# Optimization experiments

Hardware: AMD Instinct MI355X
Metric: run time of the kernel (lower is better)

The kernel has to match this reference:

```python
import jax, jax.numpy as jnp
import numpy as np

BIG_K = 13
EPS = 1e-5  # torch BatchNorm2d default


def setup_inputs() -> dict:
    key = jax.random.key(0)
    k1, k2, k3, k4 = jax.random.split(key, 4)
    B, C1, C2, H, W_ = 8, 256, 256, 64, 64
    x = jax.random.normal(k1, (B, C1, H, W_), dtype=jnp.float32)
    # scale kernel by fan-in so pre-BN activations are O(1)
    fan_in = C1 * BIG_K * BIG_K
    W = jax.random.normal(k2, (C2, C1, BIG_K, BIG_K), dtype=jnp.float32) / np.sqrt(fan_in)
    gamma = jnp.ones((C2,), dtype=jnp.float32)
    beta = jnp.zeros((C2,), dtype=jnp.float32)
    running_mean = jax.random.normal(k3, (C2,), dtype=jnp.float32) * 0.1
    running_var = jax.random.uniform(k4, (C2,), dtype=jnp.float32, minval=0.5, maxval=1.5)
    return {"x": x, "W": W, "gamma": gamma, "beta": beta,
            "running_mean": running_mean, "running_var": running_var}


def reference(x, W, gamma, beta, running_mean, running_var):
    # Fallback path of ShiftWiseConv: big-kernel conv (no bias) -> BN (inference) -> SiLU
    pad = BIG_K // 2
    y = jax.lax.conv_general_dilated(
        x, W,
        window_strides=(1, 1),
        padding=[(pad, pad), (pad, pad)],
        dimension_numbers=("NCHW", "OIHW", "NCHW"),
    )
    inv = gamma * jax.lax.rsqrt(running_var + EPS)  # [C2]
    y = y * inv[None, :, None, None] + (beta - running_mean * inv)[None, :, None, None]
    return jax.nn.silu(y)
```

## Files before the change

kernel.cpp:

```cpp
#include <hip/hip_runtime.h>
#include <stdint.h>

#define EPS 1e-5f

typedef __attribute__((ext_vector_type(8))) __bf16 bf16x8;
typedef __attribute__((ext_vector_type(16))) float f32x16;

__device__ __forceinline__ int swz4(int r) { return (r ^ (r >> 2)) & 3; }

__device__ __forceinline__ unsigned short f2bf(float f) {
  union { float f; unsigned u; } v; v.f = f;
  unsigned r = v.u + 0x7fffu + ((v.u >> 16) & 1u);
  return (unsigned short)(r >> 16);
}

__device__ __forceinline__ void glds16(const unsigned short* g, unsigned short* l) {
  __builtin_amdgcn_global_load_lds(
      (const __attribute__((address_space(1))) void*)g,
      (__attribute__((address_space(3))) void*)l, 16, 0, 0);
}
__device__ __forceinline__ void glds4(const unsigned short* g, unsigned short* l) {
  __builtin_amdgcn_global_load_lds(
      (const __attribute__((address_space(1))) void*)g,
      (__attribute__((address_space(3))) void*)l, 4, 0, 0);
}

template <int N>
__device__ __forceinline__ void vmwait() {
  asm volatile("s_waitcnt vmcnt(%0)" ::"n"(N) : "memory");
}

__global__ __launch_bounds__(256) void pack_w_kernel(
    const float* __restrict__ W, unsigned short* __restrict__ Wp) {
  const int blk = blockIdx.x;
  const int c2 = blk / 13, kh = blk - c2 * 13;
  const int c1 = threadIdx.x;
  const int c2t = c2 >> 7, m = c2 & 127;
  const int c1c = c1 >> 5, c1i = c1 & 31;
  const float* src = W + (((size_t)(c2 * 256 + c1)) * 13 + kh) * 13;
  const int rowoff = (((c1i >> 3) ^ swz4(m)) << 3) + (c1i & 7);
#pragma unroll
  for (int kw = 0; kw < 13; ++kw) {
    const int ks = (kh * 8 + c1c) * 13 + kw;
    const size_t dst = (((size_t)c2t * 1352 + ks) * 128 + m) * 32 + rowoff;
    Wp[dst] = f2bf(src[kw]);
  }
}

__global__ __launch_bounds__(256) void pack_xt_kernel(
    const float* __restrict__ x, unsigned short* __restrict__ xT) {
  const int blk = blockIdx.x;
  const int rowp = blk % 76;
  const int bc = blk / 76;
  const int c1c = bc & 7, b = bc >> 3;
  const int row = rowp - 6;
  const bool rok = (unsigned)row < 64u;
  unsigned short* dst = xT + (size_t)blk * 2560;
  const float* srcb = x + (size_t)(b * 256 + c1c * 32) * 4096 +
                      (rok ? row * 64 : 0);
#pragma unroll
  for (int e = 0; e < 10; ++e) {
    const int idx = e * 256 + threadIdx.x;
    const int colp = idx >> 5, c1i = idx & 31;
    const int ic = colp - 8;
    const float v = (rok && (unsigned)ic < 64u) ? srcb[(size_t)c1i * 4096 + ic] : 0.f;
    dst[colp * 32 + ((((c1i >> 3) ^ swz4(colp)) << 3)) + (c1i & 7)] = f2bf(v);
  }
}

__global__ __launch_bounds__(256, 2) void conv10_kernel(
    const unsigned short* __restrict__ Wp, const unsigned short* __restrict__ xT,
    const float* __restrict__ gamma, const float* __restrict__ beta,
    const float* __restrict__ mean, const float* __restrict__ var,
    float* __restrict__ out) {
  __shared__ __align__(16) unsigned short Abuf[3][8192];
  __shared__ __align__(16) unsigned short Wbuf[2][5120];
  __shared__ float s_scale[128], s_shift[128];

  const int tid = threadIdx.x;
  const int bid = blockIdx.x;
  const int b = bid & 7;
  const int h0 = ((bid >> 3) & 31) * 2;
  const int c2t = bid >> 8;

  const int wid = tid >> 6, lane = tid & 63;
  const int wr = wid >> 1, wc = wid & 1;
  const int l31 = lane & 31, hi2 = lane >> 5;

  if (tid < 128) {
    const int c2 = c2t * 128 + tid;
    const float inv = gamma[c2] * rsqrtf(var[c2] + EPS);
    s_scale[tid] = inv;
    s_shift[tid] = beta[c2] - mean[c2] * inv;
  }

  int aoffs[2][2];
#pragma unroll
  for (int mt = 0; mt < 2; ++mt)
#pragma unroll
    for (int ks = 0; ks < 2; ++ks) {
      const int m = wr * 64 + mt * 32 + l31;
      aoffs[mt][ks] = m * 64 + (((ks * 2 + hi2) ^ swz4(m)) << 4);
    }
  int ndh[2], nwl[2];
#pragma unroll
  for (int nt = 0; nt < 2; ++nt) {
    const int n = wc * 64 + nt * 32 + l31;
    ndh[nt] = n >> 6;
    nwl[nt] = n & 63;
  }

  const int tid8 = tid * 8, tid2 = tid * 2;
  const int widA = wid * 512, wid128 = wid * 128;

  const size_t c2base = (size_t)c2t * 1352;
  const int bc8 = b * 8;
  const char* Abase = (const char*)&Abuf[0][0];
  unsigned short* AbaseU = &Abuf[0][0];

  auto wtile = [&](int T) -> const unsigned short* {
    const int kh = T >> 3, c1c = T & 7;
    return xT + (size_t)((bc8 + c1c) * 76 + h0 + kh) * 2560;
  };

  f32x16 acc[2][2];
#pragma unroll
  for (int i = 0; i < 2; ++i)
#pragma unroll
    for (int j = 0; j < 2; ++j)
#pragma unroll
      for (int r = 0; r < 16; ++r) acc[i][j][r] = 0.f;

  bf16x8 rA[2][2][2], rB[2][2][2];

  int aRd = 0, aMid = 16384, aWr = 32768;

  {
    const unsigned short* at0 = Wp + (c2base << 12);
    const unsigned short* at1 = Wp + ((c2base + 1) << 12);
    glds16(at0 + tid8, AbaseU + widA);
    glds16(at0 + 2048 + tid8, AbaseU + 2048 + widA);
    glds16(at1 + tid8, AbaseU + 4096 + widA);
    glds16(at1 + 2048 + tid8, AbaseU + 6144 + widA);
    const unsigned short* ws = wtile(0);
    glds16(ws + tid8, &Wbuf[0][0] + widA);
    glds16(ws + 2048 + tid8, &Wbuf[0][2048] + widA);
    glds4(ws + 4096 + tid2, &Wbuf[0][4096] + wid128);
    glds4(ws + 4608 + tid2, &Wbuf[0][4608] + wid128);
    const unsigned short* at2 = Wp + ((c2base + 2) << 12);
    const unsigned short* at3 = Wp + ((c2base + 3) << 12);
    unsigned short* ad1 = AbaseU + 8192;
    glds16(at2 + tid8, ad1 + widA);
    glds16(at2 + 2048 + tid8, ad1 + 2048 + widA);
    glds16(at3 + tid8, ad1 + 4096 + widA);
    glds16(at3 + 2048 + tid8, ad1 + 6144 + widA);
    vmwait<4>();
    __builtin_amdgcn_s_barrier();
    __builtin_amdgcn_sched_barrier(0);
  }

#define PHASE(PH, KWA, WBA, KWB, WBB, WRT, WSRCP, WDB)                        \
  {                                                                           \
        \
    {                                                                         \
      const char* abA = Abase + aRd;                                          \
      const char* abB = abA + 8192;                                           \
      const char* wbA = (const char*)&Wbuf[(WBA)][0];                         \
      const char* wbB = (const char*)&Wbuf[(WBB)][0];                         \
      _Pragma("unroll") for (int ks = 0; ks < 2; ++ks) {                      \
        rA[0][ks][0] = *(const bf16x8*)(abA + aoffs[0][ks]);                  \
        rA[0][ks][1] = *(const bf16x8*)(abA + aoffs[1][ks]);                  \
        rA[1][ks][0] = *(const bf16x8*)(abB + aoffs[0][ks]);                  \
        rA[1][ks][1] = *(const bf16x8*)(abB + aoffs[1][ks]);                  \
        _Pragma("unroll") for (int nt = 0; nt < 2; ++nt) {                    \
          const int colA = nwl[nt] + (KWA) + 2;                               \
          rB[0][ks][nt] = *(const bf16x8*)(                                   \
              wbA + (ndh[nt] * 80 + colA) * 64 +                              \
              (((ks * 2 + hi2) ^ swz4(colA)) << 4));                          \
          const int colB = nwl[nt] + (KWB) + 2;                               \
          rB[1][ks][nt] = *(const bf16x8*)(                                   \
              wbB + (ndh[nt] * 80 + colB) * 64 +                              \
              (((ks * 2 + hi2) ^ swz4(colB)) << 4));                          \
        }                                                                     \
      }                                                                       \
    }                                                                         \
                                              \
    if ((WRT) == 1) glds16((WSRCP) + tid8, &Wbuf[(WDB)][0] + widA);           \
    if ((WRT) == 2)                                                           \
      glds16((WSRCP) + 2048 + tid8, &Wbuf[(WDB)][2048] + widA);               \
    if ((WRT) == 3) {                                                         \
      glds4((WSRCP) + 4096 + tid2, &Wbuf[(WDB)][4096] + wid128);              \
      glds4((WSRCP) + 4608 + tid2, &Wbuf[(WDB)][4608] + wid128);              \
    }                                                                         \
        \
    {                                                                         \
      int sn0 = S0 + 2 * (PH) + 4;                                            \
      if (sn0 >= 1352) sn0 -= 1352;                                           \
      int sn1 = sn0 + 1;                                                      \
      if (sn1 >= 1352) sn1 -= 1352;                                           \
      const unsigned short* at0 = Wp + ((c2base + (size_t)sn0) << 12);        \
      const unsigned short* at1 = Wp + ((c2base + (size_t)sn1) << 12);        \
      unsigned short* ad = AbaseU + (aWr >> 1);                               \
      glds16(at0 + tid8, ad + widA);                                          \
      glds16(at0 + 2048 + tid8, ad + 2048 + widA);                            \
      glds16(at1 + tid8, ad + 4096 + widA);                                   \
      glds16(at1 + 2048 + tid8, ad + 6144 + widA);                            \
    }                                                                         \
    asm volatile("" ::: "memory");                                            \
    __builtin_amdgcn_s_barrier();                                             \
    __builtin_amdgcn_sched_barrier(0);                                        \
                                         \
    {                                                                         \
      __builtin_amdgcn_s_setprio(1);                                          \
      _Pragma("unroll") for (int s = 0; s < 2; ++s)                           \
          _Pragma("unroll") for (int ks = 0; ks < 2; ++ks) {                  \
        acc[0][0] = __builtin_amdgcn_mfma_f32_32x32x16_bf16(                  \
            rA[s][ks][0], rB[s][ks][0], acc[0][0], 0, 0, 0);                  \
        acc[0][1] = __builtin_amdgcn_mfma_f32_32x32x16_bf16(                  \
            rA[s][ks][0], rB[s][ks][1], acc[0][1], 0, 0, 0);                  \
        acc[1][0] = __builtin_amdgcn_mfma_f32_32x32x16_bf16(                  \
            rA[s][ks][1], rB[s][ks][0], acc[1][0], 0, 0, 0);                  \
        acc[1][1] = __builtin_amdgcn_mfma_f32_32x32x16_bf16(                  \
            rA[s][ks][1], rB[s][ks][1], acc[1][1], 0, 0, 0);                  \
      }                                                                       \
      __builtin_amdgcn_s_setprio(0);                                          \
    }                                                                         \
             \
    vmwait<((WRT) == 0 ? 4 : ((WRT) == 3 ? 6 : 5))>();                        \
    __builtin_amdgcn_s_barrier();                                             \
    { const int t_ = aRd; aRd = aMid; aMid = aWr; aWr = t_; }                 \
  }

  for (int u = 0; u < 26; ++u) {
    const int S0 = u * 52;
    const int Tb = u * 4;
    const unsigned short* wt1 = wtile(Tb + 1);
    const unsigned short* wt2 = wtile(Tb + 2);
    const unsigned short* wt3 = wtile(Tb + 3);
    const unsigned short* wt4 = wtile((Tb + 4 == 104) ? 0 : Tb + 4);
    PHASE(0, 0, 0, 1, 0, 0, wt1, 1)
    PHASE(1, 2, 0, 3, 0, 0, wt1, 1)
    PHASE(2, 4, 0, 5, 0, 0, wt1, 1)
    PHASE(3, 6, 0, 7, 0, 1, wt1, 1)
    PHASE(4, 8, 0, 9, 0, 2, wt1, 1)
    PHASE(5, 10, 0, 11, 0, 3, wt1, 1)
    PHASE(6, 12, 0, 0, 1, 0, wt1, 1)
    PHASE(7, 1, 1, 2, 1, 0, wt2, 0)
    PHASE(8, 3, 1, 4, 1, 0, wt2, 0)
    PHASE(9, 5, 1, 6, 1, 1, wt2, 0)
    PHASE(10, 7, 1, 8, 1, 2, wt2, 0)
    PHASE(11, 9, 1, 10, 1, 3, wt2, 0)
    PHASE(12, 11, 1, 12, 1, 0, wt2, 0)
    PHASE(13, 0, 0, 1, 0, 0, wt3, 1)
    PHASE(14, 2, 0, 3, 0, 0, wt3, 1)
    PHASE(15, 4, 0, 5, 0, 0, wt3, 1)
    PHASE(16, 6, 0, 7, 0, 1, wt3, 1)
    PHASE(17, 8, 0, 9, 0, 2, wt3, 1)
    PHASE(18, 10, 0, 11, 0, 3, wt3, 1)
    PHASE(19, 12, 0, 0, 1, 0, wt3, 1)
    PHASE(20, 1, 1, 2, 1, 0, wt4, 0)
    PHASE(21, 3, 1, 4, 1, 0, wt4, 0)
    PHASE(22, 5, 1, 6, 1, 1, wt4, 0)
    PHASE(23, 7, 1, 8, 1, 2, wt4, 0)
    PHASE(24, 9, 1, 10, 1, 3, wt4, 0)
    PHASE(25, 11, 1, 12, 1, 0, wt4, 0)
  }
#undef PHASE

  vmwait<0>();

#pragma unroll
  for (int mt = 0; mt < 2; ++mt) {
#pragma unroll
    for (int nt = 0; nt < 2; ++nt) {
      const int n = wc * 64 + nt * 32 + l31;
      const int hh = h0 + (n >> 6), ww = n & 63;
#pragma unroll
      for (int r = 0; r < 16; ++r) {
        const int mloc = (r & 3) + 8 * (r >> 2) + 4 * hi2;
        const int c2l = wr * 64 + mt * 32 + mloc;
        const float y = acc[mt][nt][r] * s_scale[c2l] + s_shift[c2l];
        out[((size_t)(b * 256 + c2t * 128 + c2l)) * 4096 + hh * 64 + ww] =
            y / (1.f + __expf(-y));
      }
    }
  }
}

__global__ void naive_conv_kernel(
    const float* __restrict__ x, const float* __restrict__ W,
    const float* __restrict__ gamma, const float* __restrict__ beta,
    const float* __restrict__ mean, const float* __restrict__ var,
    float* __restrict__ out) {
  const int idx = blockIdx.x * 256 + threadIdx.x;
  if (idx >= 8 * 256 * 64 * 64) return;
  const int w = idx & 63, h = (idx >> 6) & 63;
  const int c2 = (idx >> 12) & 255, b = idx >> 20;
  float s = 0.f;
  for (int c1 = 0; c1 < 256; ++c1) {
    const float* xp = x + ((size_t)(b * 256 + c1) * 4096);
    const float* wp = W + ((size_t)(c2 * 256 + c1) * 169);
    for (int kh = 0; kh < 13; ++kh) {
      const int r = h + kh - 6;
      if ((unsigned)r >= 64u) continue;
      for (int kw = 0; kw < 13; ++kw) {
        const int c = w + kw - 6;
        if ((unsigned)c >= 64u) continue;
        s += xp[r * 64 + c] * wp[kh * 13 + kw];
      }
    }
  }
  const float inv = gamma[c2] * rsqrtf(var[c2] + EPS);
  const float y = s * inv + (beta[c2] - mean[c2] * inv);
  out[idx] = y / (1.f + __expf(-y));
}

extern "C" void kernel_launch(void* const* d_in, const int* in_sizes, int n_in,
                              void* d_out, int out_size, void* d_ws, size_t ws_size,
                              hipStream_t stream) {
  const float* x = (const float*)d_in[0];
  const float* W = (const float*)d_in[1];
  const float* gamma = (const float*)d_in[2];
  const float* beta = (const float*)d_in[3];
  const float* mean = (const float*)d_in[4];
  const float* var = (const float*)d_in[5];
  float* out = (float*)d_out;

  const size_t WP_BYTES = (size_t)256 * 43264 * 2;
  const size_t XT_BYTES = (size_t)12455424 * 2;

  if (ws_size >= WP_BYTES + XT_BYTES) {
    unsigned short* Wp = (unsigned short*)d_ws;
    unsigned short* xT = (unsigned short*)((char*)d_ws + WP_BYTES);
    pack_w_kernel<<<256 * 13, 256, 0, stream>>>(W, Wp);
    pack_xt_kernel<<<8 * 8 * 76, 256, 0, stream>>>(x, xT);
    conv10_kernel<<<512, 256, 0, stream>>>(Wp, xT, gamma, beta, mean, var, out);
  } else {
    naive_conv_kernel<<<(8 * 256 * 64 * 64 + 255) / 256, 256, 0, stream>>>(
        x, W, gamma, beta, mean, var, out);
  }
}
```

Before: 615.2 us.

## Double-buffer MFMA operand registers to overlap LDS reads with compute

Adds a register-level software pipeline. Each phase now loads the LDS fragments for the next phase into one of two register sets while issuing MFMAs on the set loaded in the previous phase. The prologue preloads three A stages and the first fragments, the A prefetch distance grows by one phase, and the W-tile write schedule shifts by one phase to match. The goal is to hide LDS read latency behind matrix math, at the cost of doubled operand registers, which under launch_bounds(256,2) may cause spilling or occupancy pressure.

```diff
diff --git a/kernel.cpp b/kernel.cpp
--- a/kernel.cpp
+++ b/kernel.cpp
@@ -68,7 +68,7 @@
   }
 }
 
-__global__ __launch_bounds__(256, 2) void conv10_kernel(
+__global__ __launch_bounds__(256, 2) void conv11_kernel(
     const unsigned short* __restrict__ Wp, const unsigned short* __restrict__ xT,
     const float* __restrict__ gamma, const float* __restrict__ beta,
     const float* __restrict__ mean, const float* __restrict__ var,
@@ -131,60 +131,93 @@
 #pragma unroll
       for (int r = 0; r < 16; ++r) acc[i][j][r] = 0.f;
 
-  bf16x8 rA[2][2][2], rB[2][2][2];
-
-  int aRd = 0, aMid = 16384, aWr = 32768;
+  bf16x8 rE_A[2][2][2], rE_B[2][2][2], rO_A[2][2][2], rO_B[2][2][2];
+
+  int aCur = 0, aNext = 16384, aNN = 32768;
 
   {
-    const unsigned short* at0 = Wp + (c2base << 12);
-    const unsigned short* at1 = Wp + ((c2base + 1) << 12);
-    glds16(at0 + tid8, AbaseU + widA);
-    glds16(at0 + 2048 + tid8, AbaseU + 2048 + widA);
-    glds16(at1 + tid8, AbaseU + 4096 + widA);
-    glds16(at1 + 2048 + tid8, AbaseU + 6144 + widA);
     const unsigned short* ws = wtile(0);
     glds16(ws + tid8, &Wbuf[0][0] + widA);
     glds16(ws + 2048 + tid8, &Wbuf[0][2048] + widA);
     glds4(ws + 4096 + tid2, &Wbuf[0][4096] + wid128);
     glds4(ws + 4608 + tid2, &Wbuf[0][4608] + wid128);
-    const unsigned short* at2 = Wp + ((c2base + 2) << 12);
-    const unsigned short* at3 = Wp + ((c2base + 3) << 12);
-    unsigned short* ad1 = AbaseU + 8192;
-    glds16(at2 + tid8, ad1 + widA);
-    glds16(at2 + 2048 + tid8, ad1 + 2048 + widA);
-    glds16(at3 + tid8, ad1 + 4096 + widA);
-    glds16(at3 + 2048 + tid8, ad1 + 6144 + widA);
-    vmwait<4>();
+#pragma unroll
+    for (int ph = 0; ph < 3; ++ph) {
+      const unsigned short* at0 = Wp + ((c2base + 2 * ph) << 12);
+      const unsigned short* at1 = Wp + ((c2base + 2 * ph + 1) << 12);
+      unsigned short* ad = AbaseU + ph * 8192;
+      glds16(at0 + tid8, ad + widA);
+      glds16(at0 + 2048 + tid8, ad + 2048 + widA);
+      glds16(at1 + tid8, ad + 4096 + widA);
+      glds16(at1 + 2048 + tid8, ad + 6144 + widA);
+    }
+    vmwait<0>();
+    __builtin_amdgcn_s_barrier();
+    const char* abA = Abase;
+    const char* abB = Abase + 8192;
+    const char* wb0 = (const char*)&Wbuf[0][0];
+#pragma unroll
+    for (int ks = 0; ks < 2; ++ks) {
+      rE_A[0][ks][0] = *(const bf16x8*)(abA + aoffs[0][ks]);
+      rE_A[0][ks][1] = *(const bf16x8*)(abA + aoffs[1][ks]);
+      rE_A[1][ks][0] = *(const bf16x8*)(abB + aoffs[0][ks]);
+      rE_A[1][ks][1] = *(const bf16x8*)(abB + aoffs[1][ks]);
+#pragma unroll
+      for (int nt = 0; nt < 2; ++nt) {
+        const int cA = nwl[nt] + 0 + 2;
+        rE_B[0][ks][nt] = *(const bf16x8*)(wb0 + (ndh[nt] * 80 + cA) * 64 +
+                                           (((ks * 2 + hi2) ^ swz4(cA)) << 4));
+        const int cB = nwl[nt] + 1 + 2;
+        rE_B[1][ks][nt] = *(const bf16x8*)(wb0 + (ndh[nt] * 80 + cB) * 64 +
+                                           (((ks * 2 + hi2) ^ swz4(cB)) << 4));
+      }
+    }
+    asm volatile("s_waitcnt lgkmcnt(0)" ::: "memory");
     __builtin_amdgcn_s_barrier();
     __builtin_amdgcn_sched_barrier(0);
   }
 
-#define PHASE(PH, KWA, WBA, KWB, WBB, WRT, WSRCP, WDB)                        \
+#define PHASE(PH, RCA, RCB, RNA, RNB, NKWA, NWBA, NKWB, NWBB, WRT, WSRCP, WDB)\
   {                                                                           \
-        \
+    __builtin_amdgcn_s_setprio(1);                                            \
+                 \
     {                                                                         \
-      const char* abA = Abase + aRd;                                          \
+      const char* abA = Abase + aNext;                                        \
       const char* abB = abA + 8192;                                           \
-      const char* wbA = (const char*)&Wbuf[(WBA)][0];                         \
-      const char* wbB = (const char*)&Wbuf[(WBB)][0];                         \
+      const char* wbA = (const char*)&Wbuf[(NWBA)][0];                        \
+      const char* wbB = (const char*)&Wbuf[(NWBB)][0];                        \
       _Pragma("unroll") for (int ks = 0; ks < 2; ++ks) {                      \
-        rA[0][ks][0] = *(const bf16x8*)(abA + aoffs[0][ks]);                  \
-        rA[0][ks][1] = *(const bf16x8*)(abA + aoffs[1][ks]);                  \
-        rA[1][ks][0] = *(const bf16x8*)(abB + aoffs[0][ks]);                  \
-        rA[1][ks][1] = *(const bf16x8*)(abB + aoffs[1][ks]);                  \
+        RNA[0][ks][0] = *(const bf16x8*)(abA + aoffs[0][ks]);                 \
+        RNA[0][ks][1] = *(const bf16x8*)(abA + aoffs[1][ks]);                 \
+        RNA[1][ks][0] = *(const bf16x8*)(abB + aoffs[0][ks]);                 \
+        RNA[1][ks][1] = *(const bf16x8*)(abB + aoffs[1][ks]);                 \
         _Pragma("unroll") for (int nt = 0; nt < 2; ++nt) {                    \
-          const int colA = nwl[nt] + (KWA) + 2;                               \
-          rB[0][ks][nt] = *(const bf16x8*)(                                   \
-              wbA + (ndh[nt] * 80 + colA) * 64 +                              \
-              (((ks * 2 + hi2) ^ swz4(colA)) << 4));                          \
-          const int colB = nwl[nt] + (KWB) + 2;                               \
-          rB[1][ks][nt] = *(const bf16x8*)(                                   \
-              wbB + (ndh[nt] * 80 + colB) * 64 +                              \
-              (((ks * 2 + hi2) ^ swz4(colB)) << 4));                          \
+          const int cA = nwl[nt] + (NKWA) + 2;                                \
+          RNB[0][ks][nt] = *(const bf16x8*)(                                  \
+              wbA + (ndh[nt] * 80 + cA) * 64 +                                \
+              (((ks * 2 + hi2) ^ swz4(cA)) << 4));                            \
+          const int cB = nwl[nt] + (NKWB) + 2;                                \
+          RNB[1][ks][nt] = *(const bf16x8*)(                                  \
+              wbB + (ndh[nt] * 80 + cB) * 64 +                                \
+              (((ks * 2 + hi2) ^ swz4(cB)) << 4));                            \
         }                                                                     \
       }                                                                       \
     }                                                                         \
-                                              \
+             \
+    _Pragma("unroll") for (int s = 0; s < 2; ++s)                             \
+        _Pragma("unroll") for (int ks = 0; ks < 2; ++ks) {                    \
+      acc[0][0] = __builtin_amdgcn_mfma_f32_32x32x16_bf16(                    \
+          RCA[s][ks][0], RCB[s][ks][0], acc[0][0], 0, 0, 0);                  \
+      acc[0][1] = __builtin_amdgcn_mfma_f32_32x32x16_bf16(                    \
+          RCA[s][ks][0], RCB[s][ks][1], acc[0][1], 0, 0, 0);                  \
+      acc[1][0] = __builtin_amdgcn_mfma_f32_32x32x16_bf16(                    \
+          RCA[s][ks][1], RCB[s][ks][0], acc[1][0], 0, 0, 0);                  \
+      acc[1][1] = __builtin_amdgcn_mfma_f32_32x32x16_bf16(                    \
+          RCA[s][ks][1], RCB[s][ks][1], acc[1][1], 0, 0, 0);                  \
+    }                                                                         \
+    __builtin_amdgcn_s_setprio(0);                                            \
+    asm volatile("s_waitcnt lgkmcnt(0)" ::: "memory");   \
+                                               \
     if ((WRT) == 1) glds16((WSRCP) + tid8, &Wbuf[(WDB)][0] + widA);           \
     if ((WRT) == 2)                                                           \
       glds16((WSRCP) + 2048 + tid8, &Wbuf[(WDB)][2048] + widA);               \
@@ -192,43 +225,24 @@
       glds4((WSRCP) + 4096 + tid2, &Wbuf[(WDB)][4096] + wid128);              \
       glds4((WSRCP) + 4608 + tid2, &Wbuf[(WDB)][4608] + wid128);              \
     }                                                                         \
-        \
+      \
     {                                                                         \
-      int sn0 = S0 + 2 * (PH) + 4;                                            \
+      int sn0 = S0 + 2 * (PH) + 6;                                            \
       if (sn0 >= 1352) sn0 -= 1352;                                           \
       int sn1 = sn0 + 1;                                                      \
       if (sn1 >= 1352) sn1 -= 1352;                                           \
       const unsigned short* at0 = Wp + ((c2base + (size_t)sn0) << 12);        \
       const unsigned short* at1 = Wp + ((c2base + (size_t)sn1) << 12);        \
-      unsigned short* ad = AbaseU + (aWr >> 1);                               \
+      unsigned short* ad = AbaseU + (aCur >> 1);                              \
       glds16(at0 + tid8, ad + widA);                                          \
       glds16(at0 + 2048 + tid8, ad + 2048 + widA);                            \
       glds16(at1 + tid8, ad + 4096 + widA);                                   \
       glds16(at1 + 2048 + tid8, ad + 6144 + widA);                            \
     }                                                                         \
-    asm volatile("" ::: "memory");                                            \
+    vmwait<((WRT) == 0 ? 4 : ((WRT) == 3 ? 6 : 5))>();                        \
     __builtin_amdgcn_s_barrier();                                             \
     __builtin_amdgcn_sched_barrier(0);                                        \
-                                         \
-    {                                                                         \
-      __builtin_amdgcn_s_setprio(1);                                          \
-      _Pragma("unroll") for (int s = 0; s < 2; ++s)                           \
-          _Pragma("unroll") for (int ks = 0; ks < 2; ++ks) {                  \
-        acc[0][0] = __builtin_amdgcn_mfma_f32_32x32x16_bf16(                  \
-            rA[s][ks][0], rB[s][ks][0], acc[0][0], 0, 0, 0);                  \
-        acc[0][1] = __builtin_amdgcn_mfma_f32_32x32x16_bf16(                  \
-            rA[s][ks][0], rB[s][ks][1], acc[0][1], 0, 0, 0);                  \
-        acc[1][0] = __builtin_amdgcn_mfma_f32_32x32x16_bf16(                  \
-            rA[s][ks][1], rB[s][ks][0], acc[1][0], 0, 0, 0);                  \
-        acc[1][1] = __builtin_amdgcn_mfma_f32_32x32x16_bf16(                  \
-            rA[s][ks][1], rB[s][ks][1], acc[1][1], 0, 0, 0);                  \
-      }                                                                       \
-      __builtin_amdgcn_s_setprio(0);                                          \
-    }                                                                         \
-             \
-    vmwait<((WRT) == 0 ? 4 : ((WRT) == 3 ? 6 : 5))>();                        \
-    __builtin_amdgcn_s_barrier();                                             \
-    { const int t_ = aRd; aRd = aMid; aMid = aWr; aWr = t_; }                 \
+    { const int t_ = aCur; aCur = aNext; aNext = aNN; aNN = t_; }             \
   }
 
   for (int u = 0; u < 26; ++u) {
@@ -238,32 +252,32 @@
     const unsigned short* wt2 = wtile(Tb + 2);
     const unsigned short* wt3 = wtile(Tb + 3);
     const unsigned short* wt4 = wtile((Tb + 4 == 104) ? 0 : Tb + 4);
-    PHASE(0, 0, 0, 1, 0, 0, wt1, 1)
-    PHASE(1, 2, 0, 3, 0, 0, wt1, 1)
-    PHASE(2, 4, 0, 5, 0, 0, wt1, 1)
-    PHASE(3, 6, 0, 7, 0, 1, wt1, 1)
-    PHASE(4, 8, 0, 9, 0, 2, wt1, 1)
-    PHASE(5, 10, 0, 11, 0, 3, wt1, 1)
-    PHASE(6, 12, 0, 0, 1, 0, wt1, 1)
-    PHASE(7, 1, 1, 2, 1, 0, wt2, 0)
-    PHASE(8, 3, 1, 4, 1, 0, wt2, 0)
-    PHASE(9, 5, 1, 6, 1, 1, wt2, 0)
-    PHASE(10, 7, 1, 8, 1, 2, wt2, 0)
-    PHASE(11, 9, 1, 10, 1, 3, wt2, 0)
-    PHASE(12, 11, 1, 12, 1, 0, wt2, 0)
-    PHASE(13, 0, 0, 1, 0, 0, wt3, 1)
-    PHASE(14, 2, 0, 3, 0, 0, wt3, 1)
-    PHASE(15, 4, 0, 5, 0, 0, wt3, 1)
-    PHASE(16, 6, 0, 7, 0, 1, wt3, 1)
-    PHASE(17, 8, 0, 9, 0, 2, wt3, 1)
-    PHASE(18, 10, 0, 11, 0, 3, wt3, 1)
-    PHASE(19, 12, 0, 0, 1, 0, wt3, 1)
-    PHASE(20, 1, 1, 2, 1, 0, wt4, 0)
-    PHASE(21, 3, 1, 4, 1, 0, wt4, 0)
-    PHASE(22, 5, 1, 6, 1, 1, wt4, 0)
-    PHASE(23, 7, 1, 8, 1, 2, wt4, 0)
-    PHASE(24, 9, 1, 10, 1, 3, wt4, 0)
-    PHASE(25, 11, 1, 12, 1, 0, wt4, 0)
+    PHASE(0, rE_A, rE_B, rO_A, rO_B, 2, 0, 3, 0, 0, wt1, 1)
+    PHASE(1, rO_A, rO_B, rE_A, rE_B, 4, 0, 5, 0, 1, wt1, 1)
+    PHASE(2, rE_A, rE_B, rO_A, rO_B, 6, 0, 7, 0, 2, wt1, 1)
+    PHASE(3, rO_A, rO_B, rE_A, rE_B, 8, 0, 9, 0, 3, wt1, 1)
+    PHASE(4, rE_A, rE_B, rO_A, rO_B, 10, 0, 11, 0, 0, wt1, 1)
+    PHASE(5, rO_A, rO_B, rE_A, rE_B, 12, 0, 0, 1, 0, wt1, 1)
+    PHASE(6, rE_A, rE_B, rO_A, rO_B, 1, 1, 2, 1, 0, wt1, 1)
+    PHASE(7, rO_A, rO_B, rE_A, rE_B, 3, 1, 4, 1, 1, wt2, 0)
+    PHASE(8, rE_A, rE_B, rO_A, rO_B, 5, 1, 6, 1, 2, wt2, 0)
+    PHASE(9, rO_A, rO_B, rE_A, rE_B, 7, 1, 8, 1, 3, wt2, 0)
+    PHASE(10, rE_A, rE_B, rO_A, rO_B, 9, 1, 10, 1, 0, wt2, 0)
+    PHASE(11, rO_A, rO_B, rE_A, rE_B, 11, 1, 12, 1, 0, wt2, 0)
+    PHASE(12, rE_A, rE_B, rO_A, rO_B, 0, 0, 1, 0, 0, wt2, 0)
+    PHASE(13, rO_A, rO_B, rE_A, rE_B, 2, 0, 3, 0, 0, wt3, 1)
+    PHASE(14, rE_A, rE_B, rO_A, rO_B, 4, 0, 5, 0, 1, wt3, 1)
+    PHASE(15, rO_A, rO_B, rE_A, rE_B, 6, 0, 7, 0, 2, wt3, 1)
+    PHASE(16, rE_A, rE_B, rO_A, rO_B, 8, 0, 9, 0, 3, wt3, 1)
+    PHASE(17, rO_A, rO_B, rE_A, rE_B, 10, 0, 11, 0, 0, wt3, 1)
+    PHASE(18, rE_A, rE_B, rO_A, rO_B, 12, 0, 0, 1, 0, wt3, 1)
+    PHASE(19, rO_A, rO_B, rE_A, rE_B, 1, 1, 2, 1, 0, wt3, 1)
+    PHASE(20, rE_A, rE_B, rO_A, rO_B, 3, 1, 4, 1, 1, wt4, 0)
+    PHASE(21, rO_A, rO_B, rE_A, rE_B, 5, 1, 6, 1, 2, wt4, 0)
+    PHASE(22, rE_A, rE_B, rO_A, rO_B, 7, 1, 8, 1, 3, wt4, 0)
+    PHASE(23, rO_A, rO_B, rE_A, rE_B, 9, 1, 10, 1, 0, wt4, 0)
+    PHASE(24, rE_A, rE_B, rO_A, rO_B, 11, 1, 12, 1, 0, wt4, 0)
+    PHASE(25, rO_A, rO_B, rE_A, rE_B, 0, 0, 1, 0, 0, wt4, 0)
   }
 #undef PHASE
 
@@ -334,7 +348,7 @@
     unsigned short* xT = (unsigned short*)((char*)d_ws + WP_BYTES);
     pack_w_kernel<<<256 * 13, 256, 0, stream>>>(W, Wp);
     pack_xt_kernel<<<8 * 8 * 76, 256, 0, stream>>>(x, xT);
-    conv10_kernel<<<512, 256, 0, stream>>>(Wp, xT, gamma, beta, mean, var, out);
+    conv11_kernel<<<512, 256, 0, stream>>>(Wp, xT, gamma, beta, mean, var, out);
   } else {
     naive_conv_kernel<<<(8 * 256 * 64 * 64 + 255) / 256, 256, 0, stream>>>(
         x, W, gamma, beta, mean, var, out);
```

Result: no change. 607.9 us (median of 2 runs) (-1.2%).
